# Kernel optimization log

Hardware: AMD Instinct MI355X
Metric: run time of the kernel (lower is better)

## Reference

```python
import jax, jax.numpy as jnp
import numpy as np

R, CIN, HF, WF = 16, 256, 128, 128   # instances, feat channels, feature map HxW
HC, WC = 128, 128                    # coarse uncertainty grid
CH = 256                             # MLP hidden / positional encoding channels
SCALE = 0.25


def setup_inputs() -> dict:
    key = jax.random.key(0)
    ks = jax.random.split(key, 11)
    s = 0.05
    return {
        "coarse_logits": jax.random.normal(ks[0], (R, 1, HC, WC), jnp.float32),
        "features": jax.random.normal(ks[1], (R, CIN, HF, WF), jnp.float32),
        "pe_gauss": jax.random.normal(ks[2], (2, CH // 2), jnp.float32),
        "W0": jax.random.normal(ks[3], (CIN + CH, CH), jnp.float32) * s,
        "b0": jnp.zeros((CH,), jnp.float32),
        "W1": jax.random.normal(ks[4], (CH, CH), jnp.float32) * s,
        "b1": jnp.zeros((CH,), jnp.float32),
        "W2": jax.random.normal(ks[5], (CH, CH), jnp.float32) * s,
        "b2": jnp.zeros((CH,), jnp.float32),
        "W3": jax.random.normal(ks[6], (CH, 1), jnp.float32) * s,
        "b3": jnp.zeros((1,), jnp.float32),
        "num_points": 8192,
    }


def _grid_sample_bilinear(feat, gx, gy):
    """F.grid_sample bilinear, align_corners=False, zero padding.
    feat: (R,C,H,W); gx,gy: (R,P) in [-1,1]. Returns (R,C,P)."""
    Rn, C, H, W = feat.shape
    x = ((gx + 1.0) * W - 1.0) * 0.5
    y = ((gy + 1.0) * H - 1.0) * 0.5
    x0 = jnp.floor(x)
    y0 = jnp.floor(y)
    wx1 = x - x0
    wy1 = y - y0
    x0i = x0.astype(jnp.int32)
    y0i = y0.astype(jnp.int32)
    flat = feat.reshape(Rn, C, H * W)

    def corner(ix, iy, w):
        valid = (ix >= 0) & (ix < W) & (iy >= 0) & (iy < H)
        lin = jnp.clip(iy, 0, H - 1) * W + jnp.clip(ix, 0, W - 1)  # (R,P)
        g = jnp.take_along_axis(
            flat, jnp.broadcast_to(lin[:, None, :], (Rn, C, lin.shape[1])), axis=2)
        return g * (w * valid.astype(feat.dtype))[:, None, :]

    return (corner(x0i, y0i, (1 - wx1) * (1 - wy1))
            + corner(x0i + 1, y0i, wx1 * (1 - wy1))
            + corner(x0i, y0i + 1, (1 - wx1) * wy1)
            + corner(x0i + 1, y0i + 1, wx1 * wy1))


def reference(coarse_logits, features, pe_gauss, W0, b0, W1, b1, W2, b2, W3, b3, num_points):
    # 1) uncertainty = -|logit| (class-agnostic, C==1 path)
    unc = -jnp.abs(coarse_logits)  # (R,1,HC,WC)
    P = min(HC * WC, num_points)
    _, idx = jax.lax.top_k(unc.reshape(R, HC * WC), P)  # (R,P)

    # 2) grid-cell-center coords of selected points, in [0,1]
    px = 0.5 / WC + (idx % WC).astype(jnp.float32) / WC
    py = 0.5 / HC + (idx // WC).astype(jnp.float32) / HC

    # 3) coordinate remap from point_sample_fine_grained_features:
    #    image_shape = [W/s-1, H/s-1]; coords*(dim-1) then /dim
    fx = (WF / SCALE - 2.0) / (WF / SCALE - 1.0)
    fy = (HF / SCALE - 2.0) / (HF / SCALE - 1.0)
    gx = 2.0 * px * fx - 1.0
    gy = 2.0 * py * fy - 1.0
    pf = _grid_sample_bilinear(features, gx, gy)  # (R,CIN,P)

    # 4) Fourier positional encoding of 2*coords-1
    loc = jnp.stack([px, py], axis=-1) * 2.0 - 1.0  # (R,P,2)
    proj = (2.0 * np.pi) * jnp.einsum('rpt,tc->rpc', loc, pe_gauss)  # (R,P,CH/2)
    pe = jnp.concatenate([jnp.sin(proj), jnp.cos(proj)], axis=-1)    # (R,P,CH)

    # 5) per-point MLP on [pos_enc, point_features] (dropout in eval = identity)
    x = jnp.concatenate([pe, pf.transpose(0, 2, 1)], axis=-1)  # (R,P,CH+CIN)
    h = jax.nn.relu(x @ W0 + b0)
    h = jax.nn.relu(h @ W1 + b1)
    h = jax.nn.relu(h @ W2 + b2)
    out = h @ W3 + b3  # (R,P,1)
    return out.transpose(0, 2, 1)  # (R, num_classes, P)
```

## Files before the change

kernel.cpp:

```cpp
#include <hip/hip_runtime.h>
#include <math.h>

typedef unsigned short u16;
typedef unsigned int   u32;
typedef unsigned long long u64;
typedef __attribute__((ext_vector_type(8))) short short8;
typedef __attribute__((ext_vector_type(4))) float f32x4;

#define R_N   16
#define HW_N  16384
#define P_N   8192
#define K0    512
#define CH_N  256
#define MB    128

__device__ __forceinline__ u16 f2bf(float x) {
  u32 u = __float_as_uint(x);
  return (u16)((u + 0x7FFFu + ((u >> 16) & 1u)) >> 16);
}
__device__ __forceinline__ void split_bf(float x, u16 &h, u16 &l) {
  u16 hh = f2bf(x);
  float hf = __uint_as_float(((u32)hh) << 16);
  h = hh;
  l = f2bf(x - hf);
}

__global__ __launch_bounds__(1024) void topk_sort(const float* __restrict__ coarse,
                                                  u32* __restrict__ slin,
                                                  u32* __restrict__ srank) {
  extern __shared__ u64 key[];
  const int r = blockIdx.x;
  const int tid = threadIdx.x;
  const float* src = coarse + r * HW_N;
#pragma unroll
  for (int u = 0; u < 4; ++u) {
    const int i4 = (u * 1024 + tid) * 4;
    const float4 v = *(const float4*)(src + i4);
    key[i4 + 0] = (((u64)__float_as_uint(-fabsf(v.x))) << 32) | (u32)(i4 + 0);
    key[i4 + 1] = (((u64)__float_as_uint(-fabsf(v.y))) << 32) | (u32)(i4 + 1);
    key[i4 + 2] = (((u64)__float_as_uint(-fabsf(v.z))) << 32) | (u32)(i4 + 2);
    key[i4 + 3] = (((u64)__float_as_uint(-fabsf(v.w))) << 32) | (u32)(i4 + 3);
  }
  __syncthreads();
  for (int k = 2; k <= HW_N; k <<= 1) {
    for (int j = k >> 1; j > 0; j >>= 1) {
      int i_[8], ip_[8];
      u64 a_[8], b_[8];
#pragma unroll
      for (int u = 0; u < 8; ++u) {
        const int p = u * 1024 + tid;
        const int lo = p & (j - 1);
        const int i = ((p - lo) << 1) | lo;
        i_[u] = i; ip_[u] = i | j;
        a_[u] = key[i]; b_[u] = key[i | j];
      }
#pragma unroll
      for (int u = 0; u < 8; ++u) {
        const bool up = ((i_[u] & k) == 0);
        if ((a_[u] > b_[u]) == up) { key[i_[u]] = b_[u]; key[ip_[u]] = a_[u]; }
      }
      __syncthreads();
    }
  }
  u32 lin_r[16];
#pragma unroll
  for (int u = 0; u < 16; ++u) lin_r[u] = (u32)key[u * 1024 + tid];
  __syncthreads();
  u16* rnk = (u16*)key;
  u32* wsum  = (u32*)((char*)key + 32768);
  u32* wbase = wsum + 16;
#pragma unroll
  for (int u = 0; u < 16; ++u)
    rnk[lin_r[u]] = (u < 8) ? (u16)(u * 1024 + tid) : (u16)0xFFFF;
  __syncthreads();
  const int lane = tid & 63;
  const int w = tid >> 6;
  u32 running = 0;
  for (int it = 0; it < 16; ++it) {
    const int i = it * 1024 + tid;
    const u16 rk = rnk[i];
    const bool f = (rk != (u16)0xFFFF);
    const u64 m = __ballot(f);
    if (lane == 0) wsum[w] = (u32)__popcll(m);
    __syncthreads();
    if (tid == 0) {
      u32 s = 0;
      for (int q = 0; q < 16; ++q) { wbase[q] = s; s += wsum[q]; }
      wbase[16] = s;
    }
    __syncthreads();
    if (f) {
      const u32 pos = running + wbase[w] + (u32)__popcll(m & ((1ull << lane) - 1ull));
      slin [r * P_N + pos] = (u32)i;
      srank[r * P_N + pos] = (u32)rk;
    }
    running += wbase[16];
    __syncthreads();
  }
}

__global__ __launch_bounds__(256) void wprep(const float* __restrict__ W0,
                                             const float* __restrict__ W1,
                                             const float* __restrict__ W2,
                                             u16* __restrict__ w0h, u16* __restrict__ w0l,
                                             u16* __restrict__ w1h, u16* __restrict__ w1l,
                                             u16* __restrict__ w2h, u16* __restrict__ w2l) {
  const int t = blockIdx.x * 256 + threadIdx.x;
  if (t < 131072) {
    const int n = t >> 9, k = t & 511;
    u16 h, l; split_bf(W0[k * 256 + n], h, l);
    w0h[t] = h; w0l[t] = l;
  } else if (t < 196608) {
    const int e = t - 131072; const int n = e >> 8, k = e & 255;
    u16 h, l; split_bf(W1[k * 256 + n], h, l);
    w1h[e] = h; w1l[e] = l;
  } else {
    const int e = t - 196608; const int n = e >> 8, k = e & 255;
    u16 h, l; split_bf(W2[k * 256 + n], h, l);
    w2h[e] = h; w2l[e] = l;
  }
}


__device__ __forceinline__ void st4(u16* base, int row, int c, const u16* v) {
  const int byte = ((row << 9) + (c << 1)) ^ ((row & 7) << 4);
  const u64 pk = (u64)v[0] | ((u64)v[1] << 16) | ((u64)v[2] << 32) | ((u64)v[3] << 48);
  *(u64*)((char*)base + byte) = pk;
}

__device__ __forceinline__ void kloop(const u16* Ah, const u16* Al,
                                      const u16* __restrict__ wh,
                                      const u16* __restrict__ wl,
                                      const int wstride, const int kofs,
                                      const int Mw, const int Nw,
                                      const int lr, const int lk,
                                      f32x4 acc[4][4]) {
#pragma unroll 2
  for (int kb = 0; kb < 8; ++kb) {
    const int kk = kb * 32 + lk * 8;
    short8 ah[4], al[4];
#pragma unroll
    for (int mt = 0; mt < 4; ++mt) {
      const int row = Mw + mt * 16 + lr;
      const int byte = ((row << 9) + (kk << 1)) ^ ((row & 7) << 4);
      ah[mt] = *(const short8*)((const char*)Ah + byte);
      al[mt] = *(const short8*)((const char*)Al + byte);
    }
#pragma unroll
    for (int nt = 0; nt < 4; ++nt) {
      const int n = Nw + nt * 16 + lr;
      const short8 bh = *(const short8*)(wh + n * wstride + kofs + kk);
      const short8 bl = *(const short8*)(wl + n * wstride + kofs + kk);
#pragma unroll
      for (int mt = 0; mt < 4; ++mt) {
        acc[mt][nt] = __builtin_amdgcn_mfma_f32_16x16x32_bf16(ah[mt], bh, acc[mt][nt], 0, 0, 0);
        acc[mt][nt] = __builtin_amdgcn_mfma_f32_16x16x32_bf16(al[mt], bh, acc[mt][nt], 0, 0, 0);
        acc[mt][nt] = __builtin_amdgcn_mfma_f32_16x16x32_bf16(ah[mt], bl, acc[mt][nt], 0, 0, 0);
      }
    }
  }
}

__device__ __forceinline__ void epiH(f32x4 acc[4][4], const float* __restrict__ bias,
                                     u16* Hh, u16* Hl,
                                     const int Mw, const int Nw, const int lr, const int lk) {
#pragma unroll
  for (int nt = 0; nt < 4; ++nt) {
    const int n = Nw + nt * 16 + lr;
    const float bv = bias[n];
#pragma unroll
    for (int mt = 0; mt < 4; ++mt) {
#pragma unroll
      for (int j = 0; j < 4; ++j) {
        const int row = Mw + mt * 16 + lk * 4 + j;
        const float h = fmaxf(acc[mt][nt][j] + bv, 0.f);
        u16 hh, hl; split_bf(h, hh, hl);
        const int byte = ((row << 9) + (n << 1)) ^ ((row & 7) << 4);
        *(u16*)((char*)Hh + byte) = hh;
        *(u16*)((char*)Hl + byte) = hl;
      }
    }
  }
}

__global__ __launch_bounds__(512, 2) void fused_pts(
    const float* __restrict__ feat, const float* __restrict__ peg,
    const u16* __restrict__ w0h, const u16* __restrict__ w0l,
    const u16* __restrict__ w1h, const u16* __restrict__ w1l,
    const u16* __restrict__ w2h, const u16* __restrict__ w2l,
    const float* __restrict__ W3, const float* __restrict__ b0,
    const float* __restrict__ b1, const float* __restrict__ b2,
    const float* __restrict__ b3,
    const u32* __restrict__ slin, const u32* __restrict__ srank,
    float* __restrict__ out)
{
  extern __shared__ char smem[];
  u16* Xh = (u16*)smem;
  u16* Xl = (u16*)(smem + 65536);
  int*   moff  = (int*)(smem + 131072);
  float* mwgt  = (float*)(smem + 133120);
  u32*   mrank = (u32*)(smem + 135168);
  float* mlx   = (float*)(smem + 135680);
  float* mly   = (float*)(smem + 136192);

  const int bid = (int)blockIdx.x;
  const int swz = (bid & 7) * 128 + (bid >> 3);
  const int r = swz >> 6;
  const int tile = swz & 63;
  const int tid = threadIdx.x;

  if (tid < MB) {
    const int p = tid;
    const u32 lin = slin [r * P_N + tile * MB + p];
    const u32 rk  = srank[r * P_N + tile * MB + p];
    const int iy = (int)(lin >> 7), ix = (int)(lin & 127u);
    const float px = 0.00390625f + (float)ix * 0.0078125f;
    const float py = 0.00390625f + (float)iy * 0.0078125f;
    const float fsc = (float)(510.0 / 511.0);
    const float gx = (2.0f * px) * fsc - 1.0f;
    const float gy = (2.0f * py) * fsc - 1.0f;
    const float xx = ((gx + 1.0f) * 128.0f - 1.0f) * 0.5f;
    const float yy = ((gy + 1.0f) * 128.0f - 1.0f) * 0.5f;
    const float x0f = floorf(xx), y0f = floorf(yy);
    const float wx = xx - x0f, wy = yy - y0f;
    const int x0 = (int)x0f, y0 = (int)y0f;
    const int x1 = x0 + 1, y1 = y0 + 1;
    const int cx0 = min(max(x0, 0), 127), cx1 = min(max(x1, 0), 127);
    const int cy0 = min(max(y0, 0), 127), cy1 = min(max(y1, 0), 127);
    const int vx0 = (x0 >= 0) & (x0 < 128), vx1 = (x1 >= 0) & (x1 < 128);
    const int vy0 = (y0 >= 0) & (y0 < 128), vy1 = (y1 >= 0) & (y1 < 128);
    moff[p]           = cy0 * 128 + cx0;
    moff[MB + p]      = cy0 * 128 + cx1;
    moff[2 * MB + p]  = cy1 * 128 + cx0;
    moff[3 * MB + p]  = cy1 * 128 + cx1;
    mwgt[p]           = (1.f - wx) * (1.f - wy) * (float)(vx0 & vy0);
    mwgt[MB + p]      = wx * (1.f - wy) * (float)(vx1 & vy0);
    mwgt[2 * MB + p]  = (1.f - wx) * wy * (float)(vx0 & vy1);
    mwgt[3 * MB + p]  = wx * wy * (float)(vx1 & vy1);
    mrank[p] = rk;
    mlx[p] = 2.0f * px - 1.0f;
    mly[p] = 2.0f * py - 1.0f;
  }
  __syncthreads();

  const int wv = tid >> 6;
  const int l  = tid & 63;
  const int lr = l & 15;
  const int lk = l >> 4;
  const int Mw = (wv >> 2) * 64;
  const int Nw = (wv & 3) * 64;

  f32x4 acc[4][4];
#pragma unroll
  for (int a = 0; a < 4; ++a)
#pragma unroll
    for (int b = 0; b < 4; ++b) acc[a][b] = (f32x4){0.f, 0.f, 0.f, 0.f};

  {
    const int p = tid & 127;
    const int grp = tid >> 7;
    const float lx = mlx[p], ly = mly[p];
#pragma unroll 2
    for (int c0 = grp * 32; c0 < grp * 32 + 32; c0 += 4) {
      u16 sh[4], sl[4], qh[4], ql[4];
#pragma unroll
      for (int q = 0; q < 4; ++q) {
        const int c = c0 + q;
        const float t = lx * peg[c] + ly * peg[128 + c];
        const float sv = __builtin_amdgcn_sinf(t);
        const float cv = __builtin_amdgcn_cosf(t);
        split_bf(sv, sh[q], sl[q]);
        split_bf(cv, qh[q], ql[q]);
      }
      st4(Xh, p, c0, sh);        st4(Xl, p, c0, sl);
      st4(Xh, p, 128 + c0, qh);  st4(Xl, p, 128 + c0, ql);
    }
  }
  __syncthreads();

  kloop(Xh, Xl, w0h, w0l, K0, 0, Mw, Nw, lr, lk, acc);
  __syncthreads();

  {
    const int p = tid & 127;
    const int grp = tid >> 7;
    const float* fb = feat + (size_t)r * (256 * HW_N);
    const int o0 = moff[p], o1 = moff[MB + p], o2 = moff[2 * MB + p], o3 = moff[3 * MB + p];
    const float q0 = mwgt[p], q1 = mwgt[MB + p], q2 = mwgt[2 * MB + p], q3 = mwgt[3 * MB + p];
#pragma unroll 2
    for (int c0 = grp * 64; c0 < grp * 64 + 64; c0 += 4) {
      u16 vh[4], vl[4];
#pragma unroll
      for (int q = 0; q < 4; ++q) {
        const float* fc = fb + (size_t)(c0 + q) * HW_N;
        const float v = q0 * fc[o0] + q1 * fc[o1] + q2 * fc[o2] + q3 * fc[o3];
        split_bf(v, vh[q], vl[q]);
      }
      st4(Xh, p, c0, vh);
      st4(Xl, p, c0, vl);
    }
  }
  __syncthreads();

  kloop(Xh, Xl, w0h, w0l, K0, 256, Mw, Nw, lr, lk, acc);
  __syncthreads();
  epiH(acc, b0, Xh, Xl, Mw, Nw, lr, lk);
  __syncthreads();

#pragma unroll
  for (int a = 0; a < 4; ++a)
#pragma unroll
    for (int b = 0; b < 4; ++b) acc[a][b] = (f32x4){0.f, 0.f, 0.f, 0.f};
  kloop(Xh, Xl, w1h, w1l, CH_N, 0, Mw, Nw, lr, lk, acc);
  __syncthreads();
  epiH(acc, b1, Xh, Xl, Mw, Nw, lr, lk);
  __syncthreads();

#pragma unroll
  for (int a = 0; a < 4; ++a)
#pragma unroll
    for (int b = 0; b < 4; ++b) acc[a][b] = (f32x4){0.f, 0.f, 0.f, 0.f};
  kloop(Xh, Xl, w2h, w2l, CH_N, 0, Mw, Nw, lr, lk, acc);
  __syncthreads();
  {
    char* H2 = smem;
#pragma unroll
    for (int nt = 0; nt < 4; ++nt) {
      const int n = Nw + nt * 16 + lr;
      const float bv = b2[n];
#pragma unroll
      for (int mt = 0; mt < 4; ++mt) {
#pragma unroll
        for (int j = 0; j < 4; ++j) {
          const int row = Mw + mt * 16 + lk * 4 + j;
          const int byte = ((row << 10) + (n << 2)) ^ ((row & 7) << 4);
          *(float*)(H2 + byte) = fmaxf(acc[mt][nt][j] + bv, 0.f);
        }
      }
    }
  }
  __syncthreads();

  {
    const int p = tid >> 2;
    const int g = tid & 3;
    const char* rowp = smem + (p << 10);
    float s = 0.f;
#pragma unroll
    for (int i = 0; i < 16; ++i) {
      const int byte = ((g << 8) + (i << 4)) ^ ((p & 7) << 4);
      const f32x4 v = *(const f32x4*)(rowp + byte);
      const int c = g * 64 + i * 4;
      s += v.x * W3[c] + v.y * W3[c + 1] + v.z * W3[c + 2] + v.w * W3[c + 3];
    }
    s += __shfl_xor(s, 1);
    s += __shfl_xor(s, 2);
    if (g == 0) out[r * P_N + mrank[p]] = s + b3[0];
  }
}

extern "C" void kernel_launch(void* const* d_in, const int* in_sizes, int n_in,
                              void* d_out, int out_size, void* d_ws, size_t ws_size,
                              hipStream_t stream) {
  const float* coarse = (const float*)d_in[0];
  const float* feat   = (const float*)d_in[1];
  const float* peg    = (const float*)d_in[2];
  const float* W0 = (const float*)d_in[3];
  const float* b0 = (const float*)d_in[4];
  const float* W1 = (const float*)d_in[5];
  const float* b1 = (const float*)d_in[6];
  const float* W2 = (const float*)d_in[7];
  const float* b2 = (const float*)d_in[8];
  const float* W3 = (const float*)d_in[9];
  const float* b3 = (const float*)d_in[10];
  float* out = (float*)d_out;

  char* ws = (char*)d_ws;
  u32* slin  = (u32*)ws;
  u32* srank = (u32*)(ws + 524288);
  u16* w0h = (u16*)(ws + 1048576);
  u16* w0l = w0h + 131072;
  u16* w1h = w0l + 131072;
  u16* w1l = w1h + 65536;
  u16* w2h = w1l + 65536;
  u16* w2l = w2h + 65536;

  hipLaunchKernelGGL(wprep, dim3(1024), dim3(256), 0, stream,
                     W0, W1, W2, w0h, w0l, w1h, w1l, w2h, w2l);
  hipLaunchKernelGGL(topk_sort, dim3(R_N), dim3(1024), 131072, stream,
                     coarse, slin, srank);
  hipLaunchKernelGGL(fused_pts, dim3(1024), dim3(512), 136704, stream,
                     feat, peg, w0h, w0l, w1h, w1l, w2h, w2l,
                     W3, b0, b1, b2, b3, slin, srank, out);
}
```

Measured before the change: 861.1 us.

## Halve MLP point tile to 64 rows and pad bitonic sort shared memory

```diff
diff --git a/kernel.cpp b/kernel.cpp
--- a/kernel.cpp
+++ b/kernel.cpp
@@ -12,7 +12,7 @@
 #define P_N   8192
 #define K0    512
 #define CH_N  256
-#define MB    128
+#define MB    64
 
 __device__ __forceinline__ u16 f2bf(float x) {
   u32 u = __float_as_uint(x);
@@ -25,6 +25,7 @@
   l = f2bf(x - hf);
 }
 
+#define PAD(i) ((i) + ((i) >> 4))
 __global__ __launch_bounds__(1024) void topk_sort(const float* __restrict__ coarse,
                                                   u32* __restrict__ slin,
                                                   u32* __restrict__ srank) {
@@ -36,35 +37,38 @@
   for (int u = 0; u < 4; ++u) {
     const int i4 = (u * 1024 + tid) * 4;
     const float4 v = *(const float4*)(src + i4);
-    key[i4 + 0] = (((u64)__float_as_uint(-fabsf(v.x))) << 32) | (u32)(i4 + 0);
-    key[i4 + 1] = (((u64)__float_as_uint(-fabsf(v.y))) << 32) | (u32)(i4 + 1);
-    key[i4 + 2] = (((u64)__float_as_uint(-fabsf(v.z))) << 32) | (u32)(i4 + 2);
-    key[i4 + 3] = (((u64)__float_as_uint(-fabsf(v.w))) << 32) | (u32)(i4 + 3);
+    key[PAD(i4 + 0)] = (((u64)__float_as_uint(-fabsf(v.x))) << 32) | (u32)(i4 + 0);
+    key[PAD(i4 + 1)] = (((u64)__float_as_uint(-fabsf(v.y))) << 32) | (u32)(i4 + 1);
+    key[PAD(i4 + 2)] = (((u64)__float_as_uint(-fabsf(v.z))) << 32) | (u32)(i4 + 2);
+    key[PAD(i4 + 3)] = (((u64)__float_as_uint(-fabsf(v.w))) << 32) | (u32)(i4 + 3);
   }
   __syncthreads();
   for (int k = 2; k <= HW_N; k <<= 1) {
     for (int j = k >> 1; j > 0; j >>= 1) {
-      int i_[8], ip_[8];
+      int ia_[8], ib_[8];
       u64 a_[8], b_[8];
 #pragma unroll
       for (int u = 0; u < 8; ++u) {
         const int p = u * 1024 + tid;
         const int lo = p & (j - 1);
         const int i = ((p - lo) << 1) | lo;
-        i_[u] = i; ip_[u] = i | j;
-        a_[u] = key[i]; b_[u] = key[i | j];
+        const int ia = PAD(i), ib = PAD(i | j);
+        ia_[u] = (i & k) ? -ia - 1 : ia;
+        ib_[u] = ib;
+        a_[u] = key[ia]; b_[u] = key[ib];
       }
 #pragma unroll
       for (int u = 0; u < 8; ++u) {
-        const bool up = ((i_[u] & k) == 0);
-        if ((a_[u] > b_[u]) == up) { key[i_[u]] = b_[u]; key[ip_[u]] = a_[u]; }
+        const bool up = (ia_[u] >= 0);
+        const int ia = up ? ia_[u] : -ia_[u] - 1;
+        if ((a_[u] > b_[u]) == up) { key[ia] = b_[u]; key[ib_[u]] = a_[u]; }
       }
       __syncthreads();
     }
   }
   u32 lin_r[16];
 #pragma unroll
-  for (int u = 0; u < 16; ++u) lin_r[u] = (u32)key[u * 1024 + tid];
+  for (int u = 0; u < 16; ++u) lin_r[u] = (u32)key[PAD(u * 1024 + tid)];
   __syncthreads();
   u16* rnk = (u16*)key;
   u32* wsum  = (u32*)((char*)key + 32768);
@@ -132,7 +136,7 @@
                                       const u16* __restrict__ wh,
                                       const u16* __restrict__ wl,
                                       const int wstride, const int kofs,
-                                      const int Mw, const int Nw,
+                                      const int Nw,
                                       const int lr, const int lk,
                                       f32x4 acc[4][4]) {
 #pragma unroll 2
@@ -141,7 +145,7 @@
     short8 ah[4], al[4];
 #pragma unroll
     for (int mt = 0; mt < 4; ++mt) {
-      const int row = Mw + mt * 16 + lr;
+      const int row = mt * 16 + lr;
       const int byte = ((row << 9) + (kk << 1)) ^ ((row & 7) << 4);
       ah[mt] = *(const short8*)((const char*)Ah + byte);
       al[mt] = *(const short8*)((const char*)Al + byte);
@@ -163,7 +167,7 @@
 
 __device__ __forceinline__ void epiH(f32x4 acc[4][4], const float* __restrict__ bias,
                                      u16* Hh, u16* Hl,
-                                     const int Mw, const int Nw, const int lr, const int lk) {
+                                     const int Nw, const int lr, const int lk) {
 #pragma unroll
   for (int nt = 0; nt < 4; ++nt) {
     const int n = Nw + nt * 16 + lr;
@@ -172,7 +176,7 @@
     for (int mt = 0; mt < 4; ++mt) {
 #pragma unroll
       for (int j = 0; j < 4; ++j) {
-        const int row = Mw + mt * 16 + lk * 4 + j;
+        const int row = mt * 16 + lk * 4 + j;
         const float h = fmaxf(acc[mt][nt][j] + bv, 0.f);
         u16 hh, hl; split_bf(h, hh, hl);
         const int byte = ((row << 9) + (n << 1)) ^ ((row & 7) << 4);
@@ -183,7 +187,7 @@
   }
 }
 
-__global__ __launch_bounds__(512, 2) void fused_pts(
+__global__ __launch_bounds__(256, 2) void fused_pts(
     const float* __restrict__ feat, const float* __restrict__ peg,
     const u16* __restrict__ w0h, const u16* __restrict__ w0l,
     const u16* __restrict__ w1h, const u16* __restrict__ w1l,
@@ -196,17 +200,17 @@
 {
   extern __shared__ char smem[];
   u16* Xh = (u16*)smem;
-  u16* Xl = (u16*)(smem + 65536);
-  int*   moff  = (int*)(smem + 131072);
-  float* mwgt  = (float*)(smem + 133120);
-  u32*   mrank = (u32*)(smem + 135168);
-  float* mlx   = (float*)(smem + 135680);
-  float* mly   = (float*)(smem + 136192);
+  u16* Xl = (u16*)(smem + 32768);
+  int*   moff  = (int*)(smem + 65536);
+  float* mwgt  = (float*)(smem + 66560);
+  u32*   mrank = (u32*)(smem + 67584);
+  float* mlx   = (float*)(smem + 67840);
+  float* mly   = (float*)(smem + 68096);
 
   const int bid = (int)blockIdx.x;
-  const int swz = (bid & 7) * 128 + (bid >> 3);
-  const int r = swz >> 6;
-  const int tile = swz & 63;
+  const int swz = (bid & 7) * 256 + (bid >> 3);
+  const int r = swz >> 7;
+  const int tile = swz & 127;
   const int tid = threadIdx.x;
 
   if (tid < MB) {
@@ -247,8 +251,7 @@
   const int l  = tid & 63;
   const int lr = l & 15;
   const int lk = l >> 4;
-  const int Mw = (wv >> 2) * 64;
-  const int Nw = (wv & 3) * 64;
+  const int Nw = wv * 64;
 
   f32x4 acc[4][4];
 #pragma unroll
@@ -257,8 +260,8 @@
     for (int b = 0; b < 4; ++b) acc[a][b] = (f32x4){0.f, 0.f, 0.f, 0.f};
 
   {
-    const int p = tid & 127;
-    const int grp = tid >> 7;
+    const int p = tid & 63;
+    const int grp = tid >> 6;
     const float lx = mlx[p], ly = mly[p];
 #pragma unroll 2
     for (int c0 = grp * 32; c0 < grp * 32 + 32; c0 += 4) {
@@ -278,12 +281,12 @@
   }
   __syncthreads();
 
-  kloop(Xh, Xl, w0h, w0l, K0, 0, Mw, Nw, lr, lk, acc);
+  kloop(Xh, Xl, w0h, w0l, K0, 0, Nw, lr, lk, acc);
   __syncthreads();
 
   {
-    const int p = tid & 127;
-    const int grp = tid >> 7;
+    const int p = tid & 63;
+    const int grp = tid >> 6;
     const float* fb = feat + (size_t)r * (256 * HW_N);
     const int o0 = moff[p], o1 = moff[MB + p], o2 = moff[2 * MB + p], o3 = moff[3 * MB + p];
     const float q0 = mwgt[p], q1 = mwgt[MB + p], q2 = mwgt[2 * MB + p], q3 = mwgt[3 * MB + p];
@@ -302,25 +305,25 @@
   }
   __syncthreads();
 
-  kloop(Xh, Xl, w0h, w0l, K0, 256, Mw, Nw, lr, lk, acc);
-  __syncthreads();
-  epiH(acc, b0, Xh, Xl, Mw, Nw, lr, lk);
+  kloop(Xh, Xl, w0h, w0l, K0, 256, Nw, lr, lk, acc);
+  __syncthreads();
+  epiH(acc, b0, Xh, Xl, Nw, lr, lk);
   __syncthreads();
 
 #pragma unroll
   for (int a = 0; a < 4; ++a)
 #pragma unroll
     for (int b = 0; b < 4; ++b) acc[a][b] = (f32x4){0.f, 0.f, 0.f, 0.f};
-  kloop(Xh, Xl, w1h, w1l, CH_N, 0, Mw, Nw, lr, lk, acc);
-  __syncthreads();
-  epiH(acc, b1, Xh, Xl, Mw, Nw, lr, lk);
+  kloop(Xh, Xl, w1h, w1l, CH_N, 0, Nw, lr, lk, acc);
+  __syncthreads();
+  epiH(acc, b1, Xh, Xl, Nw, lr, lk);
   __syncthreads();
 
 #pragma unroll
   for (int a = 0; a < 4; ++a)
 #pragma unroll
     for (int b = 0; b < 4; ++b) acc[a][b] = (f32x4){0.f, 0.f, 0.f, 0.f};
-  kloop(Xh, Xl, w2h, w2l, CH_N, 0, Mw, Nw, lr, lk, acc);
+  kloop(Xh, Xl, w2h, w2l, CH_N, 0, Nw, lr, lk, acc);
   __syncthreads();
   {
     char* H2 = smem;
@@ -332,7 +335,7 @@
       for (int mt = 0; mt < 4; ++mt) {
 #pragma unroll
         for (int j = 0; j < 4; ++j) {
-          const int row = Mw + mt * 16 + lk * 4 + j;
+          const int row = mt * 16 + lk * 4 + j;
           const int byte = ((row << 10) + (n << 2)) ^ ((row & 7) << 4);
           *(float*)(H2 + byte) = fmaxf(acc[mt][nt][j] + bv, 0.f);
         }
@@ -348,9 +351,10 @@
     float s = 0.f;
 #pragma unroll
     for (int i = 0; i < 16; ++i) {
-      const int byte = ((g << 8) + (i << 4)) ^ ((p & 7) << 4);
+      const int ie = (i + g * 4 + p) & 15;
+      const int byte = ((g << 8) + (ie << 4)) ^ ((p & 7) << 4);
       const f32x4 v = *(const f32x4*)(rowp + byte);
-      const int c = g * 64 + i * 4;
+      const int c = g * 64 + ie * 4;
       s += v.x * W3[c] + v.y * W3[c + 1] + v.z * W3[c + 2] + v.w * W3[c + 3];
     }
     s += __shfl_xor(s, 1);
@@ -387,9 +391,9 @@
 
   hipLaunchKernelGGL(wprep, dim3(1024), dim3(256), 0, stream,
                      W0, W1, W2, w0h, w0l, w1h, w1l, w2h, w2l);
-  hipLaunchKernelGGL(topk_sort, dim3(R_N), dim3(1024), 131072, stream,
+  hipLaunchKernelGGL(topk_sort, dim3(R_N), dim3(1024), 139264, stream,
                      coarse, slin, srank);
-  hipLaunchKernelGGL(fused_pts, dim3(1024), dim3(512), 136704, stream,
+  hipLaunchKernelGGL(fused_pts, dim3(2048), dim3(256), 68352, stream,
                      feat, peg, w0h, w0l, w1h, w1l, w2h, w2l,
                      W3, b0, b1, b2, b3, slin, srank, out);
 }
```

New measurement: 829.1 us. -3.7%, faster.
